# Performance work log

Hardware: AMD Instinct MI355X
Metric: run time of the kernel (lower is better)

The kernel has to match this reference:

```python
import jax, jax.numpy as jnp
import numpy as np

B, N, C, H, M = 32, 256, 1024, 16, 77
DH = C // H
W = int(N ** 0.5)
MLP_H = 4 * C

def _rel_index(w):
    ch = np.arange(w)
    coords = np.stack(np.meshgrid(ch, ch, indexing='ij'))  # [2, w, w]
    cf = coords.reshape(2, -1)
    rc = (cf[:, :, None] - cf[:, None, :]).transpose(1, 2, 0).astype(np.int64)
    rc[..., 0] += w - 1
    rc[..., 1] += w - 1
    rc[..., 0] *= 2 * w - 1
    return jnp.asarray(rc.sum(-1))  # [N, N]

REL_IDX = _rel_index(W)

def setup_inputs():
    key = jax.random.key(0)
    ks = jax.random.split(key, 12)
    p = lambda k, sh: jax.random.normal(k, sh, jnp.float32) * 0.02
    return dict(
        x=jax.random.normal(ks[0], (B, N, C), jnp.float32),
        noise_level=jax.random.normal(ks[1], (B, C), jnp.float32),
        y=jax.random.normal(ks[2], (B, M, C), jnp.float32),
        W_qkv=p(ks[3], (C, 3 * C)), b_qkv=jnp.zeros((3 * C,), jnp.float32),
        W_proj=p(ks[4], (C, C)), b_proj=jnp.zeros((C,), jnp.float32),
        rel_table=p(ks[5], ((2 * W - 1) ** 2 + 3, H)),
        W_ada=p(ks[6], (C, 6 * C)), b_ada=jnp.zeros((6 * C,), jnp.float32),
        W_fc1=p(ks[7], (C, MLP_H)), b_fc1=jnp.zeros((MLP_H,), jnp.float32),
        W_fc2=p(ks[8], (MLP_H, C)), b_fc2=jnp.zeros((C,), jnp.float32),
        W_q=p(ks[9], (C, C)), W_kv=p(ks[10], (C, 2 * C)),
    )

def _ln(x):
    # LayerNorm without affine, eps=1e-6, biased variance (matches torch)
    mu = x.mean(-1, keepdims=True)
    var = x.var(-1, keepdims=True)
    return (x - mu) * jax.lax.rsqrt(var + 1e-6)

def _modulate(x, shift, scale):
    return x * (1 + scale[:, None, :]) + shift[:, None, :]

def reference(x, noise_level, y, W_qkv, b_qkv, W_proj, b_proj, rel_table,
              W_ada, b_ada, W_fc1, b_fc1, W_fc2, b_fc2, W_q, W_kv):
    ada = jax.nn.silu(noise_level) @ W_ada + b_ada  # [B, 6C]
    sh_msa, sc_msa, g_msa, sh_mlp, sc_mlp, g_mlp = jnp.split(ada, 6, axis=1)

    # --- self-attention with relative position bias (heads split as (h d)) ---
    h = _modulate(_ln(x), sh_msa, sc_msa)
    qkv = (h @ W_qkv + b_qkv).reshape(B, N, 3, H, DH)
    q, k, v = qkv[:, :, 0], qkv[:, :, 1], qkv[:, :, 2]  # [B, N, H, DH]
    bias = rel_table[REL_IDX].transpose(2, 0, 1)  # [H, N, N]
    scores = jnp.einsum('bnhd,bmhd->bhnm', q, k) * (DH ** -0.5) + bias[None]
    attn = jax.nn.softmax(scores, axis=-1)
    o = jnp.einsum('bhnm,bmhd->bnhd', attn, v).reshape(B, N, C)
    x = x + g_msa[:, None, :] * (o @ W_proj + b_proj)

    # --- cross attention; einops '(d h)' split: head index is the FAST axis ---
    q2 = (x @ W_q).reshape(B, N, DH, H)
    kv = y @ W_kv
    k2 = kv[..., :C].reshape(B, M, DH, H)
    v2 = kv[..., C:].reshape(B, M, DH, H)
    s2 = jnp.einsum('bndh,bmdh->bhnm', q2, k2) * (DH ** -0.5)
    a2 = jax.nn.softmax(s2, axis=-1)
    o2 = jnp.einsum('bhnm,bmdh->bndh', a2, v2).reshape(B, N, C)
    x = x + o2

    # --- adaLN-modulated MLP with tanh-approx GELU ---
    h = _modulate(_ln(x), sh_mlp, sc_mlp)
    h = jax.nn.gelu(h @ W_fc1 + b_fc1, approximate=True) @ W_fc2 + b_fc2
    return x + g_mlp[:, None, :] * h
```

## Files before the change

kernel.cpp:

```cpp
#include <hip/hip_runtime.h>
#include <hip/hip_bf16.h>
#include <stdint.h>

typedef __hip_bfloat16 bf16;
using bf16x8 = __attribute__((ext_vector_type(8))) short;
using f32x4  = __attribute__((ext_vector_type(4))) float;


__device__ __forceinline__ void gload_lds16(const void* g, void* l) {
  using gchar = __attribute__((address_space(1))) char;
  using lchar = __attribute__((address_space(3))) char;
  gchar* gp = reinterpret_cast<gchar*>(reinterpret_cast<uintptr_t>(g));
  lchar* lp = reinterpret_cast<lchar*>(static_cast<uint32_t>(reinterpret_cast<uintptr_t>(l)));
  __builtin_amdgcn_global_load_lds(gp, lp, 16, 0, 0);
}

__device__ __forceinline__ unsigned short f2bf_bits(float x) {
  uint32_t u = __float_as_uint(x);
  uint32_t r = (u + 0x7fffu + ((u >> 16) & 1u)) >> 16;
  return (unsigned short)r;
}

template <int PERM>
__global__ __launch_bounds__(256) void transpose_bf16(
    const float* __restrict__ W, bf16* __restrict__ Wt, int K, int N) {
  __shared__ float t[32][33];
  const int n0 = blockIdx.x * 32, k0 = blockIdx.y * 32;
  const int tx = threadIdx.x & 31, ty = threadIdx.x >> 5;
  #pragma unroll
  for (int i = ty; i < 32; i += 8) t[i][tx] = W[(size_t)(k0 + i) * N + n0 + tx];
  __syncthreads();
  #pragma unroll
  for (int i = ty; i < 32; i += 8) {
    int n = n0 + i;
    int np;
    if constexpr (PERM == 0) np = n;
    else if constexpr (PERM == 1) np = (n & 15) * 64 + (n >> 4);
    else { int base = n & 1024, m = n & 1023; np = base + (m & 15) * 64 + (m >> 4); }
    Wt[(size_t)np * K + k0 + tx] = __float2bfloat16(t[tx][i]);
  }
}

__global__ __launch_bounds__(256) void conv_y(
    const float* __restrict__ y, bf16* __restrict__ yb) {
  int i = blockIdx.x * 256 + threadIdx.x;
  float v = (i < 2464 * 1024) ? y[i] : 0.f;
  yb[i] = __float2bfloat16(v);
}

__global__ __launch_bounds__(256) void silu_pad(
    const float* __restrict__ noise, bf16* __restrict__ Apad) {
  int i = blockIdx.x * 256 + threadIdx.x;
  float v = 0.f;
  if (i < 32 * 1024) {
    float x = noise[i];
    v = x / (1.f + __expf(-x));
  }
  Apad[i] = __float2bfloat16(v);
}

__global__ __launch_bounds__(256) void ln_mod(
    const float* __restrict__ x, const float* __restrict__ ada,
    int shOff, int scOff, bf16* __restrict__ out) {
  const int row = blockIdx.x, b = row >> 8, tid = threadIdx.x;
  const float* xr = x + (size_t)row * 1024;
  float v[4], s = 0.f, ss = 0.f;
  #pragma unroll
  for (int i = 0; i < 4; ++i) {
    v[i] = xr[tid + i * 256];
    s += v[i]; ss += v[i] * v[i];
  }
  #pragma unroll
  for (int o = 32; o; o >>= 1) { s += __shfl_xor(s, o); ss += __shfl_xor(ss, o); }
  __shared__ float red[8];
  const int w = tid >> 6;
  if ((tid & 63) == 0) { red[w] = s; red[w + 4] = ss; }
  __syncthreads();
  s = red[0] + red[1] + red[2] + red[3];
  ss = red[4] + red[5] + red[6] + red[7];
  float mu = s * (1.f / 1024.f);
  float var = ss * (1.f / 1024.f) - mu * mu;
  float rstd = rsqrtf(var + 1e-6f);
  const float* adab = ada + (size_t)b * 6144;
  #pragma unroll
  for (int i = 0; i < 4; ++i) {
    int c = tid + i * 256;
    float o = (v[i] - mu) * rstd * (1.f + adab[scOff + c]) + adab[shOff + c];
    out[(size_t)row * 1024 + c] = __float2bfloat16(o);
  }
}

enum { EPI_STORE = 0, EPI_GELU = 1, EPI_PROJ = 2, EPI_OUT = 3, EPI_ADAF = 4 };

template <int EPI>
__global__ __launch_bounds__(256, 2) void gemm_bf16(
    const bf16* __restrict__ A, const bf16* __restrict__ Bt,
    int N, int K, int gx, int grpG, int xcdP,
    const float* __restrict__ bias, const float* __restrict__ ada, int adaOff,
    const float* __restrict__ resid, float* __restrict__ outF,
    bf16* __restrict__ outB) {
  __shared__ bf16 As[128 * 64];
  __shared__ bf16 Bs[128 * 64];
  const int tid = threadIdx.x;
  const int w = tid >> 6, lane = tid & 63;
  const int wr = w >> 1, wc = w & 1;
  const int lr = lane >> 4, lc = lane & 15;

  const int flat = blockIdx.x;
  const int xcd = flat & 7, j = flat >> 3;
  const int cpg = gx / grpG;
  const int grp = xcd / xcdP, par = xcd % xcdP;
  const int bx = grp * cpg + j % cpg;
  const int by = (j / cpg) * xcdP + par;
  const int mBase = by * 128, nBase = bx * 128;

  f32x4 acc[4][4];
  #pragma unroll
  for (int mi = 0; mi < 4; ++mi)
    #pragma unroll
    for (int ni = 0; ni < 4; ++ni)
      #pragma unroll
      for (int j2 = 0; j2 < 4; ++j2) acc[mi][ni][j2] = 0.f;

  const int nK = K >> 6;
  for (int ks = 0; ks < nK; ++ks) {
    const int k0 = ks << 6;
    #pragma unroll
    for (int i = 0; i < 4; ++i) {
      int t16 = w * 256 + i * 64 + lane;
      int row = t16 >> 3;
      int cL = ((t16 & 7) ^ (row & 7)) << 3;
      gload_lds16(A + (size_t)(mBase + row) * K + k0 + cL, (char*)As + t16 * 16);
      gload_lds16(Bt + (size_t)(nBase + row) * K + k0 + cL, (char*)Bs + t16 * 16);
    }
    __syncthreads();
    #pragma unroll
    for (int kk = 0; kk < 2; ++kk) {
      bf16x8 af[4], bfr[4];
      #pragma unroll
      for (int mi = 0; mi < 4; ++mi) {
        int row = wr * 64 + mi * 16 + lc;
        int byte = row * 128 + ((kk * 64 + lr * 16) ^ ((row & 7) << 4));
        af[mi] = *reinterpret_cast<const bf16x8*>((const char*)As + byte);
      }
      #pragma unroll
      for (int ni = 0; ni < 4; ++ni) {
        int row = wc * 64 + ni * 16 + lc;
        int byte = row * 128 + ((kk * 64 + lr * 16) ^ ((row & 7) << 4));
        bfr[ni] = *reinterpret_cast<const bf16x8*>((const char*)Bs + byte);
      }
      #pragma unroll
      for (int mi = 0; mi < 4; ++mi)
        #pragma unroll
        for (int ni = 0; ni < 4; ++ni)
          acc[mi][ni] = __builtin_amdgcn_mfma_f32_16x16x32_bf16(
              af[mi], bfr[ni], acc[mi][ni], 0, 0, 0);
    }
    __syncthreads();
  }

  const int rB = mBase + wr * 64, cB = nBase + wc * 64;
  #pragma unroll
  for (int mi = 0; mi < 4; ++mi) {
    #pragma unroll
    for (int ni = 0; ni < 4; ++ni) {
      #pragma unroll
      for (int j2 = 0; j2 < 4; ++j2) {
        int r = rB + mi * 16 + lr * 4 + j2;
        int c = cB + ni * 16 + lc;
        float v = acc[mi][ni][j2];
        if (bias) v += bias[c];
        if constexpr (EPI == EPI_STORE) {
          outB[(size_t)r * N + c] = __float2bfloat16(v);
        } else if constexpr (EPI == EPI_GELU) {
          float e = __expf(1.5957691216057308f * v + 0.07135481627260086f * v * v * v);
          float t = 1.f - 2.f / (e + 1.f);
          outB[(size_t)r * N + c] = __float2bfloat16(0.5f * v * (1.f + t));
        } else if constexpr (EPI == EPI_PROJ) {
          int b = r >> 8;
          float g = ada[(size_t)b * 6144 + adaOff + c];
          float o = resid[(size_t)r * 1024 + c] + g * v;
          outF[(size_t)r * 1024 + c] = o;
          outB[(size_t)r * 1024 + c] = __float2bfloat16(o);
        } else if constexpr (EPI == EPI_OUT) {
          int b = r >> 8;
          float g = ada[(size_t)b * 6144 + adaOff + c];
          outF[(size_t)r * 1024 + c] = resid[(size_t)r * 1024 + c] + g * v;
        } else {
          if (r < 32) outF[(size_t)r * N + c] = v;
        }
      }
    }
  }
}

template <int EPI>
__global__ __launch_bounds__(512, 1) void gemm8q(
    const bf16* __restrict__ A, const bf16* __restrict__ Bt,
    int N, int K, int gx, int grpG, int xcdP,
    const float* __restrict__ bias, bf16* __restrict__ outB) {
  __shared__ bf16 AS[2][2][128 * 64];
  __shared__ bf16 BS[2][2][128 * 64];
  const int tid = threadIdx.x;
  const int w = tid >> 6, lane = tid & 63;
  const int wr = w >> 2, wc = w & 3;
  const int lr = lane >> 4, lc = lane & 15;

  const int flat = blockIdx.x;
  const int xcd = flat & 7, jj = flat >> 3;
  const int cpg = gx / grpG;
  const int grp = xcd / xcdP, par_ = xcd % xcdP;
  const int bx = grp * cpg + jj % cpg;
  const int by = (jj / cpg) * xcdP + par_;
  const int mBase = by * 256, nBase = bx * 256;
  const int nT = K >> 6;

  f32x4 acc[8][4];
  #pragma unroll
  for (int mi = 0; mi < 8; ++mi)
    #pragma unroll
    for (int ni = 0; ni < 4; ++ni) acc[mi][ni] = f32x4{0.f, 0.f, 0.f, 0.f};

  auto STAGE_A = [&](int th, int h) {
    if (th >= nT) return;
    const int k0 = th << 6;
    char* dst = (char*)&AS[th & 1][h][0];
    #pragma unroll
    for (int i = 0; i < 2; ++i) {
      int ck = i * 512 + tid;
      int rr = ck >> 3, c = ck & 7;
      int grow = mBase + (rr & 63) + ((rr >> 6) << 7) + h * 64;
      gload_lds16(A + (size_t)grow * K + k0 + ((c ^ (rr & 7)) << 3), dst + ck * 16);
    }
  };
  auto STAGE_B = [&](int th, int h) {
    if (th >= nT) return;
    const int k0 = th << 6;
    char* dst = (char*)&BS[th & 1][h][0];
    #pragma unroll
    for (int i = 0; i < 2; ++i) {
      int ck = i * 512 + tid;
      int rr = ck >> 3, c = ck & 7;
      int grow = nBase + ((rr >> 5) << 6) + h * 32 + (rr & 31);
      gload_lds16(Bt + (size_t)grow * K + k0 + ((c ^ (rr & 7)) << 3), dst + ck * 16);
    }
  };

  STAGE_A(0, 0); STAGE_A(0, 1); STAGE_B(0, 0); STAGE_B(0, 1);
  STAGE_A(1, 0); STAGE_A(1, 1);

  for (int t = 0; t < nT; ++t) {
    if (t == nT - 1) { asm volatile("s_waitcnt vmcnt(0)" ::: "memory"); }
    else             { asm volatile("s_waitcnt vmcnt(4)" ::: "memory"); }
    __builtin_amdgcn_s_barrier();

    const int p = t & 1;
    const char* A0 = (const char*)&AS[p][0][0];
    const char* A1 = (const char*)&AS[p][1][0];
    const char* B0 = (const char*)&BS[p][0][0];
    const char* B1 = (const char*)&BS[p][1][0];

    bf16x8 af0[2][4], af1[2][4], bf01[2][2], bf23[2][2];

    #pragma unroll
    for (int kk = 0; kk < 2; ++kk) {
      #pragma unroll
      for (int mi = 0; mi < 4; ++mi) {
        int rr = wr * 64 + mi * 16 + lc;
        af0[kk][mi] = *reinterpret_cast<const bf16x8*>(
            A0 + rr * 128 + ((kk * 64 + lr * 16) ^ ((rr & 7) << 4)));
      }
      #pragma unroll
      for (int ni = 0; ni < 2; ++ni) {
        int rr = wc * 32 + ni * 16 + lc;
        bf01[kk][ni] = *reinterpret_cast<const bf16x8*>(
            B0 + rr * 128 + ((kk * 64 + lr * 16) ^ ((rr & 7) << 4)));
      }
    }
    STAGE_B(t + 1, 0);
    __builtin_amdgcn_s_barrier();
    asm volatile("s_waitcnt lgkmcnt(0)" ::: "memory");
    __builtin_amdgcn_sched_barrier(0);
    __builtin_amdgcn_s_setprio(1);
    #pragma unroll
    for (int kk = 0; kk < 2; ++kk)
      #pragma unroll
      for (int mi = 0; mi < 4; ++mi)
        #pragma unroll
        for (int ni = 0; ni < 2; ++ni)
          acc[mi][ni] = __builtin_amdgcn_mfma_f32_16x16x32_bf16(
              af0[kk][mi], bf01[kk][ni], acc[mi][ni], 0, 0, 0);
    __builtin_amdgcn_s_setprio(0);
    __builtin_amdgcn_s_barrier();

    #pragma unroll
    for (int kk = 0; kk < 2; ++kk)
      #pragma unroll
      for (int ni = 0; ni < 2; ++ni) {
        int rr = wc * 32 + ni * 16 + lc;
        bf23[kk][ni] = *reinterpret_cast<const bf16x8*>(
            B1 + rr * 128 + ((kk * 64 + lr * 16) ^ ((rr & 7) << 4)));
      }
    STAGE_B(t + 1, 1);
    __builtin_amdgcn_s_barrier();
    asm volatile("s_waitcnt lgkmcnt(0)" ::: "memory");
    __builtin_amdgcn_sched_barrier(0);
    __builtin_amdgcn_s_setprio(1);
    #pragma unroll
    for (int kk = 0; kk < 2; ++kk)
      #pragma unroll
      for (int mi = 0; mi < 4; ++mi)
        #pragma unroll
        for (int ni = 0; ni < 2; ++ni)
          acc[mi][ni + 2] = __builtin_amdgcn_mfma_f32_16x16x32_bf16(
              af0[kk][mi], bf23[kk][ni], acc[mi][ni + 2], 0, 0, 0);
    __builtin_amdgcn_s_setprio(0);
    __builtin_amdgcn_s_barrier();

    #pragma unroll
    for (int kk = 0; kk < 2; ++kk)
      #pragma unroll
      for (int mi = 0; mi < 4; ++mi) {
        int rr = wr * 64 + mi * 16 + lc;
        af1[kk][mi] = *reinterpret_cast<const bf16x8*>(
            A1 + rr * 128 + ((kk * 64 + lr * 16) ^ ((rr & 7) << 4)));
      }
    STAGE_A(t + 2, 0);
    __builtin_amdgcn_s_barrier();
    asm volatile("s_waitcnt lgkmcnt(0)" ::: "memory");
    __builtin_amdgcn_sched_barrier(0);
    __builtin_amdgcn_s_setprio(1);
    #pragma unroll
    for (int kk = 0; kk < 2; ++kk)
      #pragma unroll
      for (int mi = 0; mi < 4; ++mi)
        #pragma unroll
        for (int ni = 0; ni < 2; ++ni)
          acc[mi + 4][ni] = __builtin_amdgcn_mfma_f32_16x16x32_bf16(
              af1[kk][mi], bf01[kk][ni], acc[mi + 4][ni], 0, 0, 0);
    __builtin_amdgcn_s_setprio(0);
    __builtin_amdgcn_s_barrier();

    STAGE_A(t + 2, 1);
    __builtin_amdgcn_s_barrier();
    __builtin_amdgcn_s_setprio(1);
    #pragma unroll
    for (int kk = 0; kk < 2; ++kk)
      #pragma unroll
      for (int mi = 0; mi < 4; ++mi)
        #pragma unroll
        for (int ni = 0; ni < 2; ++ni)
          acc[mi + 4][ni + 2] = __builtin_amdgcn_mfma_f32_16x16x32_bf16(
              af1[kk][mi], bf23[kk][ni], acc[mi + 4][ni + 2], 0, 0, 0);
    __builtin_amdgcn_s_setprio(0);
    __builtin_amdgcn_s_barrier();
  }

  const int rB = mBase + wr * 128, cB = nBase + wc * 64;
  #pragma unroll
  for (int mi = 0; mi < 8; ++mi) {
    #pragma unroll
    for (int ni = 0; ni < 4; ++ni) {
      #pragma unroll
      for (int j2 = 0; j2 < 4; ++j2) {
        int r = rB + mi * 16 + lr * 4 + j2;
        int c = cB + ni * 16 + lc;
        float v = acc[mi][ni][j2] + bias[c];
        if constexpr (EPI == EPI_STORE) {
          outB[(size_t)r * N + c] = __float2bfloat16(v);
        } else {
          float e = __expf(1.5957691216057308f * v + 0.07135481627260086f * v * v * v);
          float t2 = 1.f - 2.f / (e + 1.f);
          outB[(size_t)r * N + c] = __float2bfloat16(0.5f * v * (1.f + t2));
        }
      }
    }
  }
}

__global__ __launch_bounds__(512, 1) void attn1_mfma(
    const bf16* __restrict__ qkv, const float* __restrict__ rel,
    bf16* __restrict__ o) {
  __shared__ bf16 Ks[256 * 64];
  __shared__ bf16 Vt[64 * 256];
  __shared__ ushort Pl[8][32 * 40];
  __shared__ float bias_s[964];

  const int tid = threadIdx.x;
  const int w = tid >> 6, lane = tid & 63;
  const int p4 = lane >> 4, c = lane & 15;
  const int bh = blockIdx.x, b = bh >> 4, h = bh & 15;
  const bf16* basep = qkv + (size_t)b * 256 * 3072 + h * 64;

  #pragma unroll
  for (int it = 0; it < 4; ++it) {
    int t16 = it * 512 + tid;
    int row = t16 >> 3;
    int sc = ((t16 & 7) ^ (row & 7)) << 3;
    gload_lds16(basep + (size_t)row * 3072 + 1024 + sc, (char*)Ks + t16 * 16);
  }
  #pragma unroll
  for (int it = 0; it < 4; ++it) {
    int i = it * 512 + tid;
    int key = i >> 3, d0 = (i & 7) * 8;
    int4 u = *reinterpret_cast<const int4*>(basep + (size_t)key * 3072 + 2048 + d0);
    const ushort* us = reinterpret_cast<const ushort*>(&u);
    #pragma unroll
    for (int j = 0; j < 8; ++j) {
      int dh = d0 + j;
      int byte = dh * 512 + ((key * 2) ^ ((dh & 7) << 4));
      *reinterpret_cast<ushort*>((char*)Vt + byte) = us[j];
    }
  }
  for (int i = tid; i < 964; i += 512) bias_s[i] = rel[i * 16 + h];

  bf16x8 qf[2][2];
  #pragma unroll
  for (int mi = 0; mi < 2; ++mi)
    #pragma unroll
    for (int s = 0; s < 2; ++s) {
      int q = w * 32 + mi * 16 + c;
      int dh = s * 32 + p4 * 8;
      int4 u = *reinterpret_cast<const int4*>(basep + (size_t)q * 3072 + dh);
      uint32_t a[4] = {(uint32_t)u.x, (uint32_t)u.y, (uint32_t)u.z, (uint32_t)u.w};
      bf16x8 r;
      #pragma unroll
      for (int t = 0; t < 4; ++t) {
        float lo = __uint_as_float(a[t] << 16) * 0.125f;
        float hi = __uint_as_float(a[t] & 0xffff0000u) * 0.125f;
        r[2 * t]     = (short)(__float_as_uint(lo) >> 16);
        r[2 * t + 1] = (short)(__float_as_uint(hi) >> 16);
      }
      qf[mi][s] = r;
    }
  __syncthreads();

  float m_run[2][4], l_run[2][4];
  f32x4 oacc[2][4];
  #pragma unroll
  for (int mi = 0; mi < 2; ++mi)
    #pragma unroll
    for (int j = 0; j < 4; ++j) {
      m_run[mi][j] = -1e30f; l_run[mi][j] = 0.f;
      oacc[mi][j] = f32x4{0.f, 0.f, 0.f, 0.f};
    }

  ushort* Pw = &Pl[w][0];
  const int colterm = p4 * 4 - c + 15;

  for (int kt = 0; kt < 8; ++kt) {
    f32x4 sacc[2][2];
    #pragma unroll
    for (int mi = 0; mi < 2; ++mi)
      #pragma unroll
      for (int nf = 0; nf < 2; ++nf) {
        int bi = ((w * 2 + mi) - (kt * 2 + nf) + 15) * 31 + colterm;
        #pragma unroll
        for (int j = 0; j < 4; ++j) sacc[mi][nf][j] = bias_s[bi + j];
      }
    #pragma unroll
    for (int nf = 0; nf < 2; ++nf) {
      int key = kt * 32 + nf * 16 + c;
      #pragma unroll
      for (int s = 0; s < 2; ++s) {
        int byte = key * 128 + (((s * 4 + p4) ^ (key & 7)) << 4);
        bf16x8 kb = *reinterpret_cast<const bf16x8*>((const char*)Ks + byte);
        #pragma unroll
        for (int mi = 0; mi < 2; ++mi)
          sacc[mi][nf] = __builtin_amdgcn_mfma_f32_16x16x32_bf16(
              qf[mi][s], kb, sacc[mi][nf], 0, 0, 0);
      }
    }
    float sf[2][4];
    #pragma unroll
    for (int mi = 0; mi < 2; ++mi)
      #pragma unroll
      for (int j = 0; j < 4; ++j) {
        float cm = fmaxf(sacc[mi][0][j], sacc[mi][1][j]);
        cm = fmaxf(cm, __shfl_xor(cm, 1));
        cm = fmaxf(cm, __shfl_xor(cm, 2));
        cm = fmaxf(cm, __shfl_xor(cm, 4));
        cm = fmaxf(cm, __shfl_xor(cm, 8));
        float nm = fmaxf(m_run[mi][j], cm);
        sf[mi][j] = __expf(m_run[mi][j] - nm);
        m_run[mi][j] = nm;
        l_run[mi][j] *= sf[mi][j];
      }
    #pragma unroll
    for (int mi = 0; mi < 2; ++mi)
      #pragma unroll
      for (int nf = 0; nf < 4; ++nf)
        #pragma unroll
        for (int j = 0; j < 4; ++j) oacc[mi][nf][j] *= sf[mi][j];
    #pragma unroll
    for (int mi = 0; mi < 2; ++mi) {
      #pragma unroll
      for (int nf = 0; nf < 2; ++nf)
        #pragma unroll
        for (int j = 0; j < 4; ++j)
          sacc[mi][nf][j] = __expf(sacc[mi][nf][j] - m_run[mi][j]);
      #pragma unroll
      for (int j = 0; j < 4; ++j) {
        float lp = sacc[mi][0][j] + sacc[mi][1][j];
        lp += __shfl_xor(lp, 1);
        lp += __shfl_xor(lp, 2);
        lp += __shfl_xor(lp, 4);
        lp += __shfl_xor(lp, 8);
        l_run[mi][j] += lp;
      }
      #pragma unroll
      for (int nf = 0; nf < 2; ++nf)
        #pragma unroll
        for (int j = 0; j < 4; ++j)
          Pw[(mi * 16 + p4 * 4 + j) * 40 + nf * 16 + c] =
              f2bf_bits(sacc[mi][nf][j]);
    }
    bf16x8 pa[2], vb[4];
    #pragma unroll
    for (int mi = 0; mi < 2; ++mi)
      pa[mi] = *reinterpret_cast<const bf16x8*>(
          (const char*)Pw + (mi * 16 + c) * 80 + p4 * 16);
    #pragma unroll
    for (int nf = 0; nf < 4; ++nf) {
      int dh = nf * 16 + c;
      int byte = dh * 512 + (((kt * 4 + p4) ^ (dh & 7)) << 4);
      vb[nf] = *reinterpret_cast<const bf16x8*>((const char*)Vt + byte);
    }
    #pragma unroll
    for (int mi = 0; mi < 2; ++mi)
      #pragma unroll
      for (int nf = 0; nf < 4; ++nf)
        oacc[mi][nf] = __builtin_amdgcn_mfma_f32_16x16x32_bf16(
            pa[mi], vb[nf], oacc[mi][nf], 0, 0, 0);
  }

  #pragma unroll
  for (int mi = 0; mi < 2; ++mi) {
    float inv[4];
    #pragma unroll
    for (int j = 0; j < 4; ++j) inv[j] = 1.f / l_run[mi][j];
    #pragma unroll
    for (int nf = 0; nf < 4; ++nf)
      #pragma unroll
      for (int j = 0; j < 4; ++j) {
        int q = w * 32 + mi * 16 + p4 * 4 + j;
        int dh = nf * 16 + c;
        o[((size_t)b * 256 + q) * 1024 + h * 64 + dh] =
            __float2bfloat16(oacc[mi][nf][j] * inv[j]);
      }
  }
}

__global__ __launch_bounds__(512, 1) void attn2_mfma(
    const bf16* __restrict__ q2, const bf16* __restrict__ kv,
    bf16* __restrict__ o2) {
  __shared__ bf16 Ks[80 * 64];
  __shared__ bf16 Vt[64 * 128];
  __shared__ ushort Pl[8][32 * 104];

  const int tid = threadIdx.x;
  const int w = tid >> 6, lane = tid & 63;
  const int p4 = lane >> 4, c = lane & 15;
  const int bh = blockIdx.x, b = bh >> 4, h = bh & 15;
  const size_t kvrow0 = (size_t)b * 77;

  {
    int t16 = tid;
    int key = t16 >> 3;
    int sc = ((t16 & 7) ^ (key & 7)) << 3;
    gload_lds16(kv + (kvrow0 + key) * 2048 + h * 64 + sc, (char*)Ks + t16 * 16);
    if (tid < 128) {
      int u16 = 512 + tid; key = u16 >> 3;
      sc = ((u16 & 7) ^ (key & 7)) << 3;
      gload_lds16(kv + (kvrow0 + key) * 2048 + h * 64 + sc, (char*)Ks + u16 * 16);
    }
  }
  for (int i = tid; i < 80 * 8; i += 512) {
    int key = i >> 3, d0 = (i & 7) * 8;
    int4 u = *reinterpret_cast<const int4*>(
        kv + (kvrow0 + key) * 2048 + 1024 + h * 64 + d0);
    const ushort* us = reinterpret_cast<const ushort*>(&u);
    #pragma unroll
    for (int j = 0; j < 8; ++j) {
      int dh = d0 + j;
      int byte = dh * 256 + ((key * 2) ^ ((dh & 7) << 4));
      *reinterpret_cast<ushort*>((char*)Vt + byte) = us[j];
    }
  }
  {
    int row = lane >> 1, colb = 160 + (lane & 1) * 16;
    *reinterpret_cast<int4*>((char*)&Pl[w][0] + row * 208 + colb) =
        int4{0, 0, 0, 0};
  }
  bf16x8 qf[2][2];
  #pragma unroll
  for (int mi = 0; mi < 2; ++mi)
    #pragma unroll
    for (int s = 0; s < 2; ++s) {
      int q = w * 32 + mi * 16 + c;
      int dh = s * 32 + p4 * 8;
      int4 u = *reinterpret_cast<const int4*>(
          q2 + ((size_t)b * 256 + q) * 1024 + h * 64 + dh);
      uint32_t a[4] = {(uint32_t)u.x, (uint32_t)u.y, (uint32_t)u.z, (uint32_t)u.w};
      bf16x8 r;
      #pragma unroll
      for (int t = 0; t < 4; ++t) {
        float lo = __uint_as_float(a[t] << 16) * 0.125f;
        float hi = __uint_as_float(a[t] & 0xffff0000u) * 0.125f;
        r[2 * t]     = (short)(__float_as_uint(lo) >> 16);
        r[2 * t + 1] = (short)(__float_as_uint(hi) >> 16);
      }
      qf[mi][s] = r;
    }
  __syncthreads();

  f32x4 sacc[2][5];
  #pragma unroll
  for (int mi = 0; mi < 2; ++mi)
    #pragma unroll
    for (int nf = 0; nf < 5; ++nf)
      sacc[mi][nf] = f32x4{0.f, 0.f, 0.f, 0.f};
  #pragma unroll
  for (int nf = 0; nf < 5; ++nf) {
    int key = nf * 16 + c;
    #pragma unroll
    for (int s = 0; s < 2; ++s) {
      int byte = key * 128 + (((s * 4 + p4) ^ (key & 7)) << 4);
      bf16x8 kb = *reinterpret_cast<const bf16x8*>((const char*)Ks + byte);
      #pragma unroll
      for (int mi = 0; mi < 2; ++mi)
        sacc[mi][nf] = __builtin_amdgcn_mfma_f32_16x16x32_bf16(
            qf[mi][s], kb, sacc[mi][nf], 0, 0, 0);
    }
  }
  if (c >= 13) {
    #pragma unroll
    for (int mi = 0; mi < 2; ++mi)
      #pragma unroll
      for (int j = 0; j < 4; ++j) sacc[mi][4][j] = -1e30f;
  }
  float lrow[2][4];
  #pragma unroll
  for (int mi = 0; mi < 2; ++mi)
    #pragma unroll
    for (int j = 0; j < 4; ++j) {
      float cm = sacc[mi][0][j];
      #pragma unroll
      for (int nf = 1; nf < 5; ++nf) cm = fmaxf(cm, sacc[mi][nf][j]);
      cm = fmaxf(cm, __shfl_xor(cm, 1));
      cm = fmaxf(cm, __shfl_xor(cm, 2));
      cm = fmaxf(cm, __shfl_xor(cm, 4));
      cm = fmaxf(cm, __shfl_xor(cm, 8));
      float lp = 0.f;
      #pragma unroll
      for (int nf = 0; nf < 5; ++nf) {
        sacc[mi][nf][j] = __expf(sacc[mi][nf][j] - cm);
        lp += sacc[mi][nf][j];
      }
      lp += __shfl_xor(lp, 1);
      lp += __shfl_xor(lp, 2);
      lp += __shfl_xor(lp, 4);
      lp += __shfl_xor(lp, 8);
      lrow[mi][j] = lp;
    }
  ushort* Pw = &Pl[w][0];
  #pragma unroll
  for (int mi = 0; mi < 2; ++mi)
    #pragma unroll
    for (int nf = 0; nf < 5; ++nf)
      #pragma unroll
      for (int j = 0; j < 4; ++j)
        Pw[(mi * 16 + p4 * 4 + j) * 104 + nf * 16 + c] =
            f2bf_bits(sacc[mi][nf][j]);
  f32x4 oacc[2][4];
  #pragma unroll
  for (int mi = 0; mi < 2; ++mi)
    #pragma unroll
    for (int nf = 0; nf < 4; ++nf) oacc[mi][nf] = f32x4{0.f, 0.f, 0.f, 0.f};
  #pragma unroll
  for (int kk = 0; kk < 3; ++kk) {
    bf16x8 pa[2], vb[4];
    #pragma unroll
    for (int mi = 0; mi < 2; ++mi)
      pa[mi] = *reinterpret_cast<const bf16x8*>(
          (const char*)Pw + (mi * 16 + c) * 208 + kk * 64 + p4 * 16);
    #pragma unroll
    for (int nf = 0; nf < 4; ++nf) {
      int dh = nf * 16 + c;
      int byte = dh * 256 + (((kk * 4 + p4) ^ (dh & 7)) << 4);
      vb[nf] = *reinterpret_cast<const bf16x8*>((const char*)Vt + byte);
    }
    #pragma unroll
    for (int mi = 0; mi < 2; ++mi)
      #pragma unroll
      for (int nf = 0; nf < 4; ++nf)
        oacc[mi][nf] = __builtin_amdgcn_mfma_f32_16x16x32_bf16(
            pa[mi], vb[nf], oacc[mi][nf], 0, 0, 0);
  }
  #pragma unroll
  for (int mi = 0; mi < 2; ++mi) {
    float inv[4];
    #pragma unroll
    for (int j = 0; j < 4; ++j) inv[j] = 1.f / lrow[mi][j];
    #pragma unroll
    for (int nf = 0; nf < 4; ++nf)
      #pragma unroll
      for (int j = 0; j < 4; ++j) {
        int q = w * 32 + mi * 16 + p4 * 4 + j;
        int dh = nf * 16 + c;
        o2[((size_t)b * 256 + q) * 1024 + h * 64 + dh] =
            __float2bfloat16(oacc[mi][nf][j] * inv[j]);
      }
  }
}

__global__ __launch_bounds__(256) void permute_add(
    const bf16* __restrict__ o2, float* __restrict__ xcur) {
  __shared__ float s_lds[1088];
  const int tid = threadIdx.x;
  const int row0 = blockIdx.x * 4;
  for (int r = 0; r < 4; ++r) {
    const int row = row0 + r;
    #pragma unroll
    for (int i = 0; i < 4; ++i) {
      int cc = i * 256 + tid;
      float v = __bfloat162float(o2[(size_t)row * 1024 + cc]);
      s_lds[cc + (cc >> 4)] = v;
    }
    __syncthreads();
    float4 add;
    #pragma unroll
    for (int t = 0; t < 4; ++t) {
      int ct = tid * 4 + t;
      int src = (ct & 15) * 64 + (ct >> 4);
      (&add.x)[t] = s_lds[src + (src >> 4)];
    }
    float4* xp = reinterpret_cast<float4*>(xcur + (size_t)row * 1024 + tid * 4);
    float4 cur = *xp;
    cur.x += add.x; cur.y += add.y; cur.z += add.z; cur.w += add.w;
    *xp = cur;
    __syncthreads();
  }
}


extern "C" void kernel_launch(void* const* d_in, const int* in_sizes, int n_in,
                              void* d_out, int out_size, void* d_ws, size_t ws_size,
                              hipStream_t stream) {
  (void)in_sizes; (void)n_in; (void)out_size; (void)ws_size;
  const float* x      = (const float*)d_in[0];
  const float* noise  = (const float*)d_in[1];
  const float* y      = (const float*)d_in[2];
  const float* W_qkv  = (const float*)d_in[3];
  const float* b_qkv  = (const float*)d_in[4];
  const float* W_proj = (const float*)d_in[5];
  const float* b_proj = (const float*)d_in[6];
  const float* rel    = (const float*)d_in[7];
  const float* W_ada  = (const float*)d_in[8];
  const float* b_ada  = (const float*)d_in[9];
  const float* W_fc1  = (const float*)d_in[10];
  const float* b_fc1  = (const float*)d_in[11];
  const float* W_fc2  = (const float*)d_in[12];
  const float* b_fc2  = (const float*)d_in[13];
  const float* W_q    = (const float*)d_in[14];
  const float* W_kv   = (const float*)d_in[15];

  char* ws = (char*)d_ws;
  size_t off = 0;
  auto alloc = [&](size_t bytes) {
    char* p = ws + off;
    off = (off + bytes + 255) & ~(size_t)255;
    return p;
  };
  float* ada   = (float*)alloc(32u * 6144 * 4);
  float* xcur  = (float*)alloc(8192u * 1024 * 4);
  bf16* WqkvT  = (bf16*)alloc(3072u * 1024 * 2);
  bf16* WprojT = (bf16*)alloc(1024u * 1024 * 2);
  bf16* WqT    = (bf16*)alloc(1024u * 1024 * 2);
  bf16* WkvT   = (bf16*)alloc(2048u * 1024 * 2);
  bf16* Wfc1T  = (bf16*)alloc(4096u * 1024 * 2);
  bf16* Wfc2T  = (bf16*)alloc(1024u * 4096 * 2);
  bf16* WadaT  = (bf16*)alloc(6144u * 1024 * 2);
  bf16* Apad   = (bf16*)alloc(128u * 1024 * 2);
  bf16* hbuf   = (bf16*)alloc(8192u * 1024 * 2);
  bf16* big    = (bf16*)alloc(8192u * 4096 * 2);
  bf16* obuf   = (bf16*)alloc(8192u * 1024 * 2);
  bf16* kvbuf  = (bf16*)alloc(2560u * 2048 * 2);
  bf16* ybuf   = (bf16*)alloc(2560u * 1024 * 2);
  float* outF  = (float*)d_out;

  transpose_bf16<0><<<dim3(96, 32), 256, 0, stream>>>(W_qkv, WqkvT, 1024, 3072);
  transpose_bf16<0><<<dim3(32, 32), 256, 0, stream>>>(W_proj, WprojT, 1024, 1024);
  transpose_bf16<1><<<dim3(32, 32), 256, 0, stream>>>(W_q, WqT, 1024, 1024);
  transpose_bf16<2><<<dim3(64, 32), 256, 0, stream>>>(W_kv, WkvT, 1024, 2048);
  transpose_bf16<0><<<dim3(128, 32), 256, 0, stream>>>(W_fc1, Wfc1T, 1024, 4096);
  transpose_bf16<0><<<dim3(32, 128), 256, 0, stream>>>(W_fc2, Wfc2T, 4096, 1024);
  transpose_bf16<0><<<dim3(192, 32), 256, 0, stream>>>(W_ada, WadaT, 1024, 6144);
  conv_y<<<2560 * 1024 / 256, 256, 0, stream>>>(y, ybuf);

  silu_pad<<<512, 256, 0, stream>>>(noise, Apad);
  gemm_bf16<EPI_ADAF><<<48, 256, 0, stream>>>(
      Apad, WadaT, 6144, 1024, 48, 8, 1, b_ada, nullptr, 0, nullptr, ada, nullptr);

  ln_mod<<<8192, 256, 0, stream>>>(x, ada, 0, 1024, hbuf);
  gemm8q<EPI_STORE><<<384, 512, 0, stream>>>(
      hbuf, WqkvT, 3072, 1024, 12, 4, 2, b_qkv, big);
  attn1_mfma<<<512, 512, 0, stream>>>(big, rel, obuf);
  gemm_bf16<EPI_PROJ><<<512, 256, 0, stream>>>(
      obuf, WprojT, 1024, 1024, 8, 1, 8, b_proj, ada, 2048, x, xcur, hbuf);

  gemm_bf16<EPI_STORE><<<512, 256, 0, stream>>>(
      hbuf, WqT, 1024, 1024, 8, 1, 8, nullptr, nullptr, 0, nullptr, nullptr, obuf);
  gemm_bf16<EPI_STORE><<<320, 256, 0, stream>>>(
      ybuf, WkvT, 2048, 1024, 16, 8, 1, nullptr, nullptr, 0, nullptr, nullptr, kvbuf);
  attn2_mfma<<<512, 512, 0, stream>>>(obuf, kvbuf, big);
  permute_add<<<2048, 256, 0, stream>>>(big, xcur);

  ln_mod<<<8192, 256, 0, stream>>>(xcur, ada, 3072, 4096, hbuf);
  gemm8q<EPI_GELU><<<512, 512, 0, stream>>>(
      hbuf, Wfc1T, 4096, 1024, 16, 4, 2, b_fc1, big);
  gemm_bf16<EPI_OUT><<<512, 256, 0, stream>>>(
      big, Wfc2T, 1024, 4096, 8, 1, 8, b_fc2, ada, 5120, xcur, outF, nullptr);
}
```

Measured before the change: 513.6 us.

## Add 256x128-tile 8-wave pipelined GEMM for N=1024 projections

Adds gemm8q2, a 512-thread GEMM with 256x128 output tiles, double-buffered direct-to-LDS loads and interleaved half-tile staging with MFMA priority hints. It supports store, GELU, projection-residual and output epilogues. It replaces the older gemm_bf16 for the attention projection, cross-attention Q projection and fc2, halving the block count to 256 with larger tiles. The aim is more data reuse per block and better load/compute overlap, at the cost of fewer blocks than CUs and so possibly poorer occupancy and load balance.

```diff
diff --git a/kernel.cpp b/kernel.cpp
--- a/kernel.cpp
+++ b/kernel.cpp
@@ -378,6 +378,183 @@
   }
 }
 
+template <int EPI>
+__global__ __launch_bounds__(512, 1) void gemm8q2(
+    const bf16* __restrict__ A, const bf16* __restrict__ Bt,
+    int N, int K, int gx, int grpG, int xcdP,
+    const float* __restrict__ bias, const float* __restrict__ ada, int adaOff,
+    const float* __restrict__ resid, float* __restrict__ outF,
+    bf16* __restrict__ outB) {
+  __shared__ bf16 AS[2][2][128 * 64];
+  __shared__ bf16 BS[2][2][64 * 64];
+  const int tid = threadIdx.x;
+  const int w = tid >> 6, lane = tid & 63;
+  const int wr = w >> 2, wc = w & 3;
+  const int lr = lane >> 4, lc = lane & 15;
+
+  const int flat = blockIdx.x;
+  const int xcd = flat & 7, jj = flat >> 3;
+  const int cpg = gx / grpG;
+  const int grp = xcd / xcdP, par_ = xcd % xcdP;
+  const int bx = grp * cpg + jj % cpg;
+  const int by = (jj / cpg) * xcdP + par_;
+  const int mBase = by * 256, nBase = bx * 128;
+  const int nT = K >> 6;
+
+  f32x4 acc[8][2];
+  #pragma unroll
+  for (int mi = 0; mi < 8; ++mi)
+    #pragma unroll
+    for (int ni = 0; ni < 2; ++ni) acc[mi][ni] = f32x4{0.f, 0.f, 0.f, 0.f};
+
+  auto STAGE_A = [&](int th, int h) {
+    if (th >= nT) return;
+    const int k0 = th << 6;
+    char* dst = (char*)&AS[th & 1][h][0];
+    #pragma unroll
+    for (int i = 0; i < 2; ++i) {
+      int ck = i * 512 + tid;
+      int rr = ck >> 3, c = ck & 7;
+      int grow = mBase + (rr & 63) + ((rr >> 6) << 7) + h * 64;
+      gload_lds16(A + (size_t)grow * K + k0 + ((c ^ (rr & 7)) << 3), dst + ck * 16);
+    }
+  };
+  auto STAGE_B = [&](int th, int h) {
+    if (th >= nT) return;
+    const int k0 = th << 6;
+    char* dst = (char*)&BS[th & 1][h][0];
+    int ck = tid;
+    int rr = ck >> 3, c = ck & 7;
+    int grow = nBase + h * 64 + rr;
+    gload_lds16(Bt + (size_t)grow * K + k0 + ((c ^ (rr & 7)) << 3), dst + ck * 16);
+  };
+
+  STAGE_A(0, 0); STAGE_A(0, 1); STAGE_B(0, 0); STAGE_B(0, 1);
+  STAGE_A(1, 0); STAGE_A(1, 1);
+
+  for (int t = 0; t < nT; ++t) {
+    if (t == nT - 1)      { asm volatile("s_waitcnt vmcnt(0)" ::: "memory"); }
+    else if (t == 0)      { asm volatile("s_waitcnt vmcnt(4)" ::: "memory"); }
+    else                  { asm volatile("s_waitcnt vmcnt(2)" ::: "memory"); }
+    __builtin_amdgcn_s_barrier();
+
+    const int p = t & 1;
+    const char* A0 = (const char*)&AS[p][0][0];
+    const char* A1 = (const char*)&AS[p][1][0];
+    const char* Bh = (const char*)&BS[p][wc >> 1][0];
+    const int rbB = (wc & 1) * 32 + lc;
+
+    bf16x8 af0[2][4], af1[2][4], bfv[2][2];
+
+    #pragma unroll
+    for (int kk = 0; kk < 2; ++kk) {
+      #pragma unroll
+      for (int mi = 0; mi < 4; ++mi) {
+        int rr = wr * 64 + mi * 16 + lc;
+        af0[kk][mi] = *reinterpret_cast<const bf16x8*>(
+            A0 + rr * 128 + ((kk * 64 + lr * 16) ^ ((rr & 7) << 4)));
+      }
+      #pragma unroll
+      for (int ni = 0; ni < 2; ++ni) {
+        int rr = rbB + ni * 16;
+        bfv[kk][ni] = *reinterpret_cast<const bf16x8*>(
+            Bh + rr * 128 + ((kk * 64 + lr * 16) ^ ((rr & 7) << 4)));
+      }
+    }
+    STAGE_B(t + 1, 0);
+    __builtin_amdgcn_s_barrier();
+    asm volatile("s_waitcnt lgkmcnt(0)" ::: "memory");
+    __builtin_amdgcn_sched_barrier(0);
+    __builtin_amdgcn_s_setprio(1);
+    #pragma unroll
+    for (int mi = 0; mi < 4; ++mi)
+      #pragma unroll
+      for (int ni = 0; ni < 2; ++ni)
+        acc[mi][ni] = __builtin_amdgcn_mfma_f32_16x16x32_bf16(
+            af0[0][mi], bfv[0][ni], acc[mi][ni], 0, 0, 0);
+    __builtin_amdgcn_s_setprio(0);
+    __builtin_amdgcn_s_barrier();
+
+    STAGE_A(t + 2, 0);
+    __builtin_amdgcn_s_barrier();
+    __builtin_amdgcn_s_setprio(1);
+    #pragma unroll
+    for (int mi = 0; mi < 4; ++mi)
+      #pragma unroll
+      for (int ni = 0; ni < 2; ++ni)
+        acc[mi][ni] = __builtin_amdgcn_mfma_f32_16x16x32_bf16(
+            af0[1][mi], bfv[1][ni], acc[mi][ni], 0, 0, 0);
+    __builtin_amdgcn_s_setprio(0);
+    __builtin_amdgcn_s_barrier();
+
+    #pragma unroll
+    for (int kk = 0; kk < 2; ++kk)
+      #pragma unroll
+      for (int mi = 0; mi < 4; ++mi) {
+        int rr = wr * 64 + mi * 16 + lc;
+        af1[kk][mi] = *reinterpret_cast<const bf16x8*>(
+            A1 + rr * 128 + ((kk * 64 + lr * 16) ^ ((rr & 7) << 4)));
+      }
+    STAGE_B(t + 1, 1);
+    __builtin_amdgcn_s_barrier();
+    asm volatile("s_waitcnt lgkmcnt(0)" ::: "memory");
+    __builtin_amdgcn_sched_barrier(0);
+    __builtin_amdgcn_s_setprio(1);
+    #pragma unroll
+    for (int mi = 0; mi < 4; ++mi)
+      #pragma unroll
+      for (int ni = 0; ni < 2; ++ni)
+        acc[mi + 4][ni] = __builtin_amdgcn_mfma_f32_16x16x32_bf16(
+            af1[0][mi], bfv[0][ni], acc[mi + 4][ni], 0, 0, 0);
+    __builtin_amdgcn_s_setprio(0);
+    __builtin_amdgcn_s_barrier();
+
+    STAGE_A(t + 2, 1);
+    __builtin_amdgcn_s_barrier();
+    __builtin_amdgcn_s_setprio(1);
+    #pragma unroll
+    for (int mi = 0; mi < 4; ++mi)
+      #pragma unroll
+      for (int ni = 0; ni < 2; ++ni)
+        acc[mi + 4][ni] = __builtin_amdgcn_mfma_f32_16x16x32_bf16(
+            af1[1][mi], bfv[1][ni], acc[mi + 4][ni], 0, 0, 0);
+    __builtin_amdgcn_s_setprio(0);
+    __builtin_amdgcn_s_barrier();
+  }
+
+  const int rB = mBase + wr * 128, cB = nBase + wc * 32;
+  #pragma unroll
+  for (int mi = 0; mi < 8; ++mi) {
+    #pragma unroll
+    for (int ni = 0; ni < 2; ++ni) {
+      #pragma unroll
+      for (int j2 = 0; j2 < 4; ++j2) {
+        int r = rB + mi * 16 + lr * 4 + j2;
+        int c = cB + ni * 16 + lc;
+        float v = acc[mi][ni][j2];
+        if (bias) v += bias[c];
+        if constexpr (EPI == EPI_STORE) {
+          outB[(size_t)r * N + c] = __float2bfloat16(v);
+        } else if constexpr (EPI == EPI_GELU) {
+          float e = __expf(1.5957691216057308f * v + 0.07135481627260086f * v * v * v);
+          float t2 = 1.f - 2.f / (e + 1.f);
+          outB[(size_t)r * N + c] = __float2bfloat16(0.5f * v * (1.f + t2));
+        } else if constexpr (EPI == EPI_PROJ) {
+          int b = r >> 8;
+          float g = ada[(size_t)b * 6144 + adaOff + c];
+          float o = resid[(size_t)r * 1024 + c] + g * v;
+          outF[(size_t)r * 1024 + c] = o;
+          outB[(size_t)r * 1024 + c] = __float2bfloat16(o);
+        } else if constexpr (EPI == EPI_OUT) {
+          int b = r >> 8;
+          float g = ada[(size_t)b * 6144 + adaOff + c];
+          outF[(size_t)r * 1024 + c] = resid[(size_t)r * 1024 + c] + g * v;
+        }
+      }
+    }
+  }
+}
+
 __global__ __launch_bounds__(512, 1) void attn1_mfma(
     const bf16* __restrict__ qkv, const float* __restrict__ rel,
     bf16* __restrict__ o) {
@@ -806,11 +983,11 @@
   gemm8q<EPI_STORE><<<384, 512, 0, stream>>>(
       hbuf, WqkvT, 3072, 1024, 12, 4, 2, b_qkv, big);
   attn1_mfma<<<512, 512, 0, stream>>>(big, rel, obuf);
-  gemm_bf16<EPI_PROJ><<<512, 256, 0, stream>>>(
-      obuf, WprojT, 1024, 1024, 8, 1, 8, b_proj, ada, 2048, x, xcur, hbuf);
-
-  gemm_bf16<EPI_STORE><<<512, 256, 0, stream>>>(
-      hbuf, WqT, 1024, 1024, 8, 1, 8, nullptr, nullptr, 0, nullptr, nullptr, obuf);
+  gemm8q2<EPI_PROJ><<<256, 512, 0, stream>>>(
+      obuf, WprojT, 1024, 1024, 8, 4, 2, b_proj, ada, 2048, x, xcur, hbuf);
+
+  gemm8q2<EPI_STORE><<<256, 512, 0, stream>>>(
+      hbuf, WqT, 1024, 1024, 8, 4, 2, nullptr, nullptr, 0, nullptr, nullptr, obuf);
   gemm_bf16<EPI_STORE><<<320, 256, 0, stream>>>(
       ybuf, WkvT, 2048, 1024, 16, 8, 1, nullptr, nullptr, 0, nullptr, nullptr, kvbuf);
   attn2_mfma<<<512, 512, 0, stream>>>(obuf, kvbuf, big);
@@ -819,6 +996,6 @@
   ln_mod<<<8192, 256, 0, stream>>>(xcur, ada, 3072, 4096, hbuf);
   gemm8q<EPI_GELU><<<512, 512, 0, stream>>>(
       hbuf, Wfc1T, 4096, 1024, 16, 4, 2, b_fc1, big);
-  gemm_bf16<EPI_OUT><<<512, 256, 0, stream>>>(
-      big, Wfc2T, 1024, 4096, 8, 1, 8, b_fc2, ada, 5120, xcur, outF, nullptr);
-}
+  gemm8q2<EPI_OUT><<<256, 512, 0, stream>>>(
+      big, Wfc2T, 1024, 4096, 8, 4, 2, b_fc2, ada, 5120, xcur, outF, nullptr);
+}
```

Measured after the change: 526.4 us. 1.02x slower.

## Merge weight-prep kernels into one launch and fuse permute-add with LayerNorm

Applied to the files above, without the earlier changes.

Nine separate prep launches (weight transposes to bf16, the y conversion and the silu padding) become one prep_all kernel that picks its work from the block index. The cross-attention permute/residual add is also fused with the following LayerNorm+modulate, so xcur is not read back from memory a second time. This cuts launch overhead and one full pass over the 32MB fp32 activation. In exchange, prep_all has runtime branches in place of templated permutations, and the fused kernel processes one row per block.

```diff
diff --git a/kernel.cpp b/kernel.cpp
--- a/kernel.cpp
+++ b/kernel.cpp
@@ -21,12 +21,49 @@
   return (unsigned short)r;
 }
 
-template <int PERM>
-__global__ __launch_bounds__(256) void transpose_bf16(
-    const float* __restrict__ W, bf16* __restrict__ Wt, int K, int N) {
+__global__ __launch_bounds__(256) void prep_all(
+    const float* __restrict__ Wqkv, const float* __restrict__ Wproj,
+    const float* __restrict__ Wq, const float* __restrict__ Wkv,
+    const float* __restrict__ Wfc1, const float* __restrict__ Wfc2,
+    const float* __restrict__ Wada, const float* __restrict__ y,
+    const float* __restrict__ noise,
+    bf16* __restrict__ WqkvT, bf16* __restrict__ WprojT,
+    bf16* __restrict__ WqT, bf16* __restrict__ WkvT,
+    bf16* __restrict__ Wfc1T, bf16* __restrict__ Wfc2T,
+    bf16* __restrict__ WadaT, bf16* __restrict__ yb, bf16* __restrict__ Apad) {
   __shared__ float t[32][33];
-  const int n0 = blockIdx.x * 32, k0 = blockIdx.y * 32;
-  const int tx = threadIdx.x & 31, ty = threadIdx.x >> 5;
+  const int tid = threadIdx.x;
+  int bid = blockIdx.x;
+
+  const float* W = nullptr; bf16* Wt = nullptr;
+  int K = 0, N = 0, nx = 0, perm = 0;
+  if (bid < 3072)        { W = Wqkv;  Wt = WqkvT;  K = 1024; N = 3072; nx = 96;  perm = 0; }
+  else if (bid < 4096)   { bid -= 3072;  W = Wproj; Wt = WprojT; K = 1024; N = 1024; nx = 32;  perm = 0; }
+  else if (bid < 5120)   { bid -= 4096;  W = Wq;    Wt = WqT;    K = 1024; N = 1024; nx = 32;  perm = 1; }
+  else if (bid < 7168)   { bid -= 5120;  W = Wkv;   Wt = WkvT;   K = 1024; N = 2048; nx = 64;  perm = 2; }
+  else if (bid < 11264)  { bid -= 7168;  W = Wfc1;  Wt = Wfc1T;  K = 1024; N = 4096; nx = 128; perm = 0; }
+  else if (bid < 15360)  { bid -= 11264; W = Wfc2;  Wt = Wfc2T;  K = 4096; N = 1024; nx = 32;  perm = 0; }
+  else if (bid < 21504)  { bid -= 15360; W = Wada;  Wt = WadaT;  K = 1024; N = 6144; nx = 192; perm = 0; }
+  else if (bid < 31744) {
+    bid -= 21504;
+    int i = bid * 256 + tid;
+    float v = (i < 2464 * 1024) ? y[i] : 0.f;
+    yb[i] = __float2bfloat16(v);
+    return;
+  } else {
+    bid -= 31744;
+    int i = bid * 256 + tid;
+    float v = 0.f;
+    if (i < 32 * 1024) {
+      float xx = noise[i];
+      v = xx / (1.f + __expf(-xx));
+    }
+    Apad[i] = __float2bfloat16(v);
+    return;
+  }
+
+  const int n0 = (bid % nx) * 32, k0 = (bid / nx) * 32;
+  const int tx = tid & 31, ty = tid >> 5;
   #pragma unroll
   for (int i = ty; i < 32; i += 8) t[i][tx] = W[(size_t)(k0 + i) * N + n0 + tx];
   __syncthreads();
@@ -34,29 +71,11 @@
   for (int i = ty; i < 32; i += 8) {
     int n = n0 + i;
     int np;
-    if constexpr (PERM == 0) np = n;
-    else if constexpr (PERM == 1) np = (n & 15) * 64 + (n >> 4);
+    if (perm == 0) np = n;
+    else if (perm == 1) np = (n & 15) * 64 + (n >> 4);
     else { int base = n & 1024, m = n & 1023; np = base + (m & 15) * 64 + (m >> 4); }
     Wt[(size_t)np * K + k0 + tx] = __float2bfloat16(t[tx][i]);
   }
-}
-
-__global__ __launch_bounds__(256) void conv_y(
-    const float* __restrict__ y, bf16* __restrict__ yb) {
-  int i = blockIdx.x * 256 + threadIdx.x;
-  float v = (i < 2464 * 1024) ? y[i] : 0.f;
-  yb[i] = __float2bfloat16(v);
-}
-
-__global__ __launch_bounds__(256) void silu_pad(
-    const float* __restrict__ noise, bf16* __restrict__ Apad) {
-  int i = blockIdx.x * 256 + threadIdx.x;
-  float v = 0.f;
-  if (i < 32 * 1024) {
-    float x = noise[i];
-    v = x / (1.f + __expf(-x));
-  }
-  Apad[i] = __float2bfloat16(v);
 }
 
 __global__ __launch_bounds__(256) void ln_mod(
@@ -86,6 +105,51 @@
   for (int i = 0; i < 4; ++i) {
     int c = tid + i * 256;
     float o = (v[i] - mu) * rstd * (1.f + adab[scOff + c]) + adab[shOff + c];
+    out[(size_t)row * 1024 + c] = __float2bfloat16(o);
+  }
+}
+
+__global__ __launch_bounds__(256) void permute_ln(
+    const bf16* __restrict__ o2, float* __restrict__ xcur,
+    const float* __restrict__ ada, int shOff, int scOff,
+    bf16* __restrict__ out) {
+  __shared__ float s_lds[1088];
+  __shared__ float red[8];
+  const int row = blockIdx.x, b = row >> 8, tid = threadIdx.x;
+  #pragma unroll
+  for (int i = 0; i < 4; ++i) {
+    int hm = i * 256 + tid;
+    float v = __bfloat162float(o2[(size_t)row * 1024 + hm]);
+    s_lds[hm + (hm >> 4)] = v;
+  }
+  __syncthreads();
+  float v[4], s = 0.f, ss = 0.f;
+  float4* xp = reinterpret_cast<float4*>(xcur + (size_t)row * 1024 + tid * 4);
+  float4 cur = *xp;
+  #pragma unroll
+  for (int tI = 0; tI < 4; ++tI) {
+    int c = tid * 4 + tI;
+    int src = (c & 15) * 64 + (c >> 4);
+    float xv = (&cur.x)[tI] + s_lds[src + (src >> 4)];
+    v[tI] = xv; s += xv; ss += xv * xv;
+  }
+  float4 nw; nw.x = v[0]; nw.y = v[1]; nw.z = v[2]; nw.w = v[3];
+  *xp = nw;
+  #pragma unroll
+  for (int o = 32; o; o >>= 1) { s += __shfl_xor(s, o); ss += __shfl_xor(ss, o); }
+  const int w = tid >> 6;
+  if ((tid & 63) == 0) { red[w] = s; red[w + 4] = ss; }
+  __syncthreads();
+  s = red[0] + red[1] + red[2] + red[3];
+  ss = red[4] + red[5] + red[6] + red[7];
+  float mu = s * (1.f / 1024.f);
+  float var = ss * (1.f / 1024.f) - mu * mu;
+  float rstd = rsqrtf(var + 1e-6f);
+  const float* adab = ada + (size_t)b * 6144;
+  #pragma unroll
+  for (int tI = 0; tI < 4; ++tI) {
+    int c = tid * 4 + tI;
+    float o = (v[tI] - mu) * rstd * (1.f + adab[scOff + c]) + adab[shOff + c];
     out[(size_t)row * 1024 + c] = __float2bfloat16(o);
   }
 }
@@ -714,35 +778,6 @@
   }
 }
 
-__global__ __launch_bounds__(256) void permute_add(
-    const bf16* __restrict__ o2, float* __restrict__ xcur) {
-  __shared__ float s_lds[1088];
-  const int tid = threadIdx.x;
-  const int row0 = blockIdx.x * 4;
-  for (int r = 0; r < 4; ++r) {
-    const int row = row0 + r;
-    #pragma unroll
-    for (int i = 0; i < 4; ++i) {
-      int cc = i * 256 + tid;
-      float v = __bfloat162float(o2[(size_t)row * 1024 + cc]);
-      s_lds[cc + (cc >> 4)] = v;
-    }
-    __syncthreads();
-    float4 add;
-    #pragma unroll
-    for (int t = 0; t < 4; ++t) {
-      int ct = tid * 4 + t;
-      int src = (ct & 15) * 64 + (ct >> 4);
-      (&add.x)[t] = s_lds[src + (src >> 4)];
-    }
-    float4* xp = reinterpret_cast<float4*>(xcur + (size_t)row * 1024 + tid * 4);
-    float4 cur = *xp;
-    cur.x += add.x; cur.y += add.y; cur.z += add.z; cur.w += add.w;
-    *xp = cur;
-    __syncthreads();
-  }
-}
-
 
 extern "C" void kernel_launch(void* const* d_in, const int* in_sizes, int n_in,
                               void* d_out, int out_size, void* d_ws, size_t ws_size,
@@ -789,16 +824,10 @@
   bf16* ybuf   = (bf16*)alloc(2560u * 1024 * 2);
   float* outF  = (float*)d_out;
 
-  transpose_bf16<0><<<dim3(96, 32), 256, 0, stream>>>(W_qkv, WqkvT, 1024, 3072);
-  transpose_bf16<0><<<dim3(32, 32), 256, 0, stream>>>(W_proj, WprojT, 1024, 1024);
-  transpose_bf16<1><<<dim3(32, 32), 256, 0, stream>>>(W_q, WqT, 1024, 1024);
-  transpose_bf16<2><<<dim3(64, 32), 256, 0, stream>>>(W_kv, WkvT, 1024, 2048);
-  transpose_bf16<0><<<dim3(128, 32), 256, 0, stream>>>(W_fc1, Wfc1T, 1024, 4096);
-  transpose_bf16<0><<<dim3(32, 128), 256, 0, stream>>>(W_fc2, Wfc2T, 4096, 1024);
-  transpose_bf16<0><<<dim3(192, 32), 256, 0, stream>>>(W_ada, WadaT, 1024, 6144);
-  conv_y<<<2560 * 1024 / 256, 256, 0, stream>>>(y, ybuf);
-
-  silu_pad<<<512, 256, 0, stream>>>(noise, Apad);
+  prep_all<<<32256, 256, 0, stream>>>(
+      W_qkv, W_proj, W_q, W_kv, W_fc1, W_fc2, W_ada, y, noise,
+      WqkvT, WprojT, WqT, WkvT, Wfc1T, Wfc2T, WadaT, ybuf, Apad);
+
   gemm_bf16<EPI_ADAF><<<48, 256, 0, stream>>>(
       Apad, WadaT, 6144, 1024, 48, 8, 1, b_ada, nullptr, 0, nullptr, ada, nullptr);
 
@@ -814,9 +843,8 @@
   gemm_bf16<EPI_STORE><<<320, 256, 0, stream>>>(
       ybuf, WkvT, 2048, 1024, 16, 8, 1, nullptr, nullptr, 0, nullptr, nullptr, kvbuf);
   attn2_mfma<<<512, 512, 0, stream>>>(obuf, kvbuf, big);
-  permute_add<<<2048, 256, 0, stream>>>(big, xcur);
-
-  ln_mod<<<8192, 256, 0, stream>>>(xcur, ada, 3072, 4096, hbuf);
+  permute_ln<<<8192, 256, 0, stream>>>(big, xcur, ada, 3072, 4096, hbuf);
+
   gemm8q<EPI_GELU><<<512, 512, 0, stream>>>(
       hbuf, Wfc1T, 4096, 1024, 16, 4, 2, b_fc1, big);
   gemm_bf16<EPI_OUT><<<512, 256, 0, stream>>>(
```

Result: faster. 489.2 us (median of 2 runs) (-4.8%).
